# Kernel tuning notes

Measured on AMD Instinct MI355X. Metric: run time of the kernel, lower is better.

## Reference

```python
import jax, jax.numpy as jnp
import numpy as np

HID = 128
EDGE_FEAT = 4
NUM_G = 20
CUTOFF = 10.0
N_NODES = 20000
N_EDGES = 640000


def setup_inputs() -> dict:
    key = jax.random.key(0)
    ks = jax.random.split(key, 20)
    s = 0.02
    in_e = 2 * HID + EDGE_FEAT + NUM_G  # 280
    inp = {
        "h": jax.random.normal(ks[0], (N_NODES, HID), jnp.float32),
        "x": jax.random.normal(ks[1], (N_NODES, 3), jnp.float32),
        "edge_attr": jax.random.normal(ks[2], (N_EDGES, EDGE_FEAT), jnp.float32),
        "edge_index": jax.random.randint(ks[3], (2, N_EDGES), 0, N_NODES, jnp.int32),
        "mask_ligand": jax.random.randint(ks[4], (N_NODES,), 0, 2, jnp.int32),
        # edge_mlp: 2 linear layers, silu after both (act_last=True)
        "W_e1": jax.random.normal(ks[5], (in_e, HID), jnp.float32) * s,
        "b_e1": jnp.zeros((HID,), jnp.float32),
        "W_e2": jax.random.normal(ks[6], (HID, HID), jnp.float32) * s,
        "b_e2": jnp.zeros((HID,), jnp.float32),
        # edge gate: Linear(hidden,1) + sigmoid
        "W_g": jax.random.normal(ks[7], (HID, 1), jnp.float32) * s,
        "b_g": jnp.zeros((1,), jnp.float32),
        # node_mlp: Linear -> silu -> Linear (no act last)
        "W_n1": jax.random.normal(ks[8], (2 * HID, HID), jnp.float32) * s,
        "b_n1": jnp.zeros((HID,), jnp.float32),
        "W_n2": jax.random.normal(ks[9], (HID, HID), jnp.float32) * s,
        "b_n2": jnp.zeros((HID,), jnp.float32),
        # x_mlp: Linear -> silu -> Linear(no bias, tiny init) -> tanh
        "W_x1": jax.random.normal(ks[10], (HID, HID), jnp.float32) * s,
        "b_x1": jnp.zeros((HID,), jnp.float32),
        "W_x2": jax.random.normal(ks[11], (HID, 1), jnp.float32) * 0.001,
    }
    return inp


def reference(h, x, edge_attr, W_e1, b_e1, W_e2, b_e2, W_g, b_g,
              W_n1, b_n1, W_n2, b_n2, W_x1, b_x1, W_x2,
              edge_index, mask_ligand):
    src, dst = edge_index[0], edge_index[1]
    rel = x[dst] - x[src]                                # [E,3]
    d2 = jnp.sum(rel * rel, axis=-1, keepdims=True)     # [E,1]
    r = jnp.sqrt(d2 + 1e-8)
    # Gaussian smearing RBF
    offset = jnp.linspace(0.0, CUTOFF, NUM_G)
    coeff = -0.5 / (offset[1] - offset[0]) ** 2
    d_feat = jnp.exp(coeff * (r - offset) ** 2)          # [E,NUM_G]
    m_in = jnp.concatenate([h[dst], h[src], d_feat, edge_attr], axis=-1)
    m = jax.nn.silu(m_in @ W_e1 + b_e1)
    m = jax.nn.silu(m @ W_e2 + b_e2)
    g = jax.nn.sigmoid(m @ W_g + b_g)                    # [E,1]
    msg = m * g
    agg = jnp.zeros((h.shape[0], HID), msg.dtype).at[dst].add(msg)
    nm = jax.nn.silu(jnp.concatenate([agg, h], axis=-1) @ W_n1 + b_n1)
    h_out = h + (nm @ W_n2 + b_n2)
    coef = jnp.tanh(jax.nn.silu(m @ W_x1 + b_x1) @ W_x2)  # [E,1]
    vec = rel / (r + 1.0) * coef
    dx = jnp.zeros_like(x).at[dst].add(vec.astype(x.dtype))
    x_out = x + dx * mask_ligand.astype(x.dtype)[:, None]
    return (h_out, x_out)
```

## Files before the change

### kernel.cpp

```cpp
#include <hip/hip_runtime.h>
#include <hip/hip_bf16.h>
#include <math.h>

#define HID 128
#define NUM_G 20
#define EF 4
#define NN 20000
#define NE 640000
#define KN1 256
#define TS 136

typedef __attribute__((ext_vector_type(8))) short short8;
typedef __attribute__((ext_vector_type(4))) short short4v;
typedef __attribute__((ext_vector_type(4))) float floatx4;
typedef __attribute__((ext_vector_type(4))) unsigned int uintx4;

__device__ __forceinline__ float silu_f(float v){
    return v * __builtin_amdgcn_rcpf(1.0f + __expf(-v));
}
__device__ __forceinline__ float sigm_f(float v){
    return __builtin_amdgcn_rcpf(1.0f + __expf(-v));
}
__device__ __forceinline__ float tanh_f(float v){
    return 1.0f - 2.0f * __builtin_amdgcn_rcpf(1.0f + __expf(2.0f * v));
}
__device__ __forceinline__ unsigned short f2bf(float v){
    unsigned int u = __float_as_uint(v);
    u = (u + 0x7fffu + ((u >> 16) & 1u)) >> 16;
    return (unsigned short)u;
}
__device__ __forceinline__ float bf2f(unsigned short u){
    return __uint_as_float(((unsigned int)u) << 16);
}
__device__ __forceinline__ unsigned int pk2(float a, float b){
    __hip_bfloat162 h = __float22bfloat162_rn(make_float2(a, b));
    return *(unsigned int*)&h;
}
__device__ __forceinline__ float2 up2(unsigned int u){
    __hip_bfloat162 h = *(__hip_bfloat162*)&u;
    return __bfloat1622float2(h);
}

__global__ __launch_bounds__(320) void prep_hist_kernel(
    const float* __restrict__ W_e1, const float* __restrict__ W_e2,
    const float* __restrict__ W_x1, const float* __restrict__ W_n1,
    const float* __restrict__ W_n2,
    unsigned short* __restrict__ WT1d, unsigned short* __restrict__ WT1s,
    unsigned short* __restrict__ WT1r,
    unsigned short* __restrict__ WT_e2, unsigned short* __restrict__ WT_x1,
    unsigned short* __restrict__ WT_n1, unsigned short* __restrict__ WT_n2,
    const int* __restrict__ edge_index, int* __restrict__ counts)
{
    int t = threadIdx.x;
    if (blockIdx.x < 128) {
        int n = blockIdx.x;
        if (t < HID) {
            WT1d[n*HID + t] = f2bf(W_e1[t*HID + n]);
            WT1s[n*HID + t] = f2bf(W_e1[(HID+t)*HID + n]);
            WT_e2[n*HID + t] = f2bf(W_e2[t*HID + n]);
            WT_x1[n*HID + t] = f2bf(W_x1[t*HID + n]);
            WT_n2[n*HID + t] = f2bf(W_n2[t*HID + n]);
        }
        if (t < 32) WT1r[n*32 + t] = (t < NUM_G+EF) ? f2bf(W_e1[(256+t)*HID + n]) : (unsigned short)0;
        if (t < KN1) WT_n1[n*KN1 + t] = f2bf(W_n1[t*HID + n]);
    } else {
        int e = (blockIdx.x - 128) * 320 + t;
        atomicAdd(&counts[edge_index[NE + e]], 1);
    }
}

__global__ __launch_bounds__(1024) void scan_kernel(
    const int* __restrict__ counts, int* __restrict__ cursor)
{
    __shared__ int part[1024];
    const int t = threadIdx.x;
    const int CH = (NN + 1023) / 1024;
    int base = t * CH;
    int s = 0;
    for (int i = 0; i < CH; ++i) { int idx = base + i; if (idx < NN) s += counts[idx]; }
    part[t] = s; __syncthreads();
    for (int off = 1; off < 1024; off <<= 1) {
        int v = (t >= off) ? part[t - off] : 0;
        __syncthreads();
        part[t] += v;
        __syncthreads();
    }
    int run = (t == 0) ? 0 : part[t - 1];
    for (int i = 0; i < CH; ++i) {
        int idx = base + i;
        if (idx < NN) { cursor[idx] = run; run += counts[idx]; }
    }
}

#define PD_BLOCKS ((NN + 63) / 64)
__global__ __launch_bounds__(256) void build_pd_kernel(
    const int* __restrict__ edge_index, const float* __restrict__ x,
    const float* __restrict__ edge_attr, int* __restrict__ cursor,
    int2* __restrict__ pair2, float4* __restrict__ geom4,
    unsigned short* __restrict__ attrb,
    const float* __restrict__ h, const float* __restrict__ b_e1,
    const unsigned short* __restrict__ WT1d, const unsigned short* __restrict__ WT1s,
    unsigned short* __restrict__ PD, unsigned short* __restrict__ PS)
{
    __shared__ __align__(16) unsigned short T[4][16*TS];

    if (blockIdx.x >= PD_BLOCKS) {
        int e = (blockIdx.x - PD_BLOCKS) * 256 + threadIdx.x;
        int s = edge_index[e];
        int d = edge_index[NE + e];
        int pos = atomicAdd(&cursor[d], 1);
        float rx = x[d*3+0] - x[s*3+0];
        float ry = x[d*3+1] - x[s*3+1];
        float rz = x[d*3+2] - x[s*3+2];
        float r  = sqrtf(rx*rx + ry*ry + rz*rz + 1e-8f);
        pair2[pos] = make_int2(s, d);
        geom4[pos] = make_float4(rx, ry, rz, r);
        short4v a;
        #pragma unroll
        for (int j = 0; j < 4; ++j) a[j] = (short)f2bf(edge_attr[(size_t)e*EF + j]);
        *(short4v*)(attrb + (size_t)pos*4) = a;
        return;
    }

    const int wv   = threadIdx.x >> 6;
    const int lane = threadIdx.x & 63;
    const int quad = lane >> 4;
    const int l15  = lane & 15;
    int node = blockIdx.x * 64 + wv * 16 + l15;
    if (node >= NN) node = NN - 1;
    unsigned short* Tw = &T[wv][0];

    short8 ah[4];
    #pragma unroll
    for (int kc = 0; kc < 4; ++kc) {
        const float* p = h + (size_t)node*HID + kc*32 + quad*8;
        float4 f0 = *(const float4*)(p);
        float4 f1 = *(const float4*)(p + 4);
        uintx4 u;
        u[0] = pk2(f0.x, f0.y); u[1] = pk2(f0.z, f0.w);
        u[2] = pk2(f1.x, f1.y); u[3] = pk2(f1.z, f1.w);
        ah[kc] = __builtin_bit_cast(short8, u);
    }

    floatx4 ad[8], as[8];
    #pragma unroll
    for (int t = 0; t < 8; ++t) { ad[t] = (floatx4){0,0,0,0}; as[t] = (floatx4){0,0,0,0}; }
    #pragma unroll
    for (int kc = 0; kc < 4; ++kc) {
        #pragma unroll
        for (int t = 0; t < 8; ++t) {
            short8 bd = *(const short8*)(WT1d + (size_t)(t*16+l15)*HID + kc*32 + quad*8);
            short8 bs = *(const short8*)(WT1s + (size_t)(t*16+l15)*HID + kc*32 + quad*8);
            ad[t] = __builtin_amdgcn_mfma_f32_16x16x32_bf16(ah[kc], bd, ad[t], 0, 0, 0);
            as[t] = __builtin_amdgcn_mfma_f32_16x16x32_bf16(ah[kc], bs, as[t], 0, 0, 0);
        }
    }
    #pragma unroll
    for (int t = 0; t < 8; ++t) {
        int col = t*16 + l15;
        float bv = b_e1[col];
        #pragma unroll
        for (int i = 0; i < 4; ++i)
            Tw[(quad*4+i)*TS + col] = f2bf(ad[t][i] + bv);
    }
    __builtin_amdgcn_wave_barrier();
    #pragma unroll
    for (int kc = 0; kc < 4; ++kc)
        *(short8*)(PD + (size_t)node*HID + kc*32 + quad*8) =
            *(const short8*)(&Tw[l15*TS + kc*32 + quad*8]);
    __builtin_amdgcn_wave_barrier();
    #pragma unroll
    for (int t = 0; t < 8; ++t) {
        int col = t*16 + l15;
        #pragma unroll
        for (int i = 0; i < 4; ++i)
            Tw[(quad*4+i)*TS + col] = f2bf(as[t][i]);
    }
    __builtin_amdgcn_wave_barrier();
    #pragma unroll
    for (int kc = 0; kc < 4; ++kc)
        *(short8*)(PS + (size_t)node*HID + kc*32 + quad*8) =
            *(const short8*)(&Tw[l15*TS + kc*32 + quad*8]);
}

__global__ __launch_bounds__(128, 3) void egnn_edge_mfma(
    const int2* __restrict__ pair2, const float4* __restrict__ geom4,
    const unsigned short* __restrict__ attrb,
    const unsigned short* __restrict__ PD, const unsigned short* __restrict__ PS,
    const unsigned short* __restrict__ WT1r,
    const unsigned short* __restrict__ WT_e2,
    const unsigned short* __restrict__ WT_x1,
    const float* __restrict__ b_e2,
    const float* __restrict__ W_g,  const float* __restrict__ b_g,
    const float* __restrict__ b_x1, const float* __restrict__ W_x2,
    float* __restrict__ agg, float* __restrict__ dxv)
{
    __shared__ __align__(16) unsigned short T[2][32*TS];
    __shared__ int   s_dst[2][33];
    __shared__ float s_g[2][32];
    __shared__ float s_vec[2][96];

    const int wv   = threadIdx.x >> 6;
    const int lane = threadIdx.x & 63;
    const int quad = lane >> 4;
    const int l15  = lane & 15;
    const int bid  = (int)(blockIdx.x & 7) * 1250 + (int)(blockIdx.x >> 3);
    const int e0   = (bid * 2 + wv) * 32;

    unsigned short* Tw = &T[wv][0];

    int   sreg = 0, dreg = 0;
    float rxr = 0.f, ryr = 0.f, rzr = 0.f, rreg = 0.f;
    if (lane < 32) {
        int2  p = pair2[e0 + lane];
        float4 g = geom4[e0 + lane];
        sreg = p.x; dreg = p.y;
        rxr = g.x; ryr = g.y; rzr = g.z; rreg = g.w;
        s_dst[wv][lane] = dreg;
    }
    if (lane == 32) s_dst[wv][32] = -1;

    const int   nd0 = __shfl(dreg, l15);
    const int   ns0 = __shfl(sreg, l15);
    const float rr0 = __shfl(rreg, l15);
    const int   nd1 = __shfl(dreg, 16 + l15);
    const int   ns1 = __shfl(sreg, 16 + l15);
    const float rr1 = __shfl(rreg, 16 + l15);

    short8 pdv0[4], psv0[4], pdv1[4], psv1[4];
    #pragma unroll
    for (int kc = 0; kc < 4; ++kc) {
        pdv0[kc] = *(const short8*)(PD + (size_t)nd0*HID + kc*32 + quad*8);
        psv0[kc] = *(const short8*)(PS + (size_t)ns0*HID + kc*32 + quad*8);
        pdv1[kc] = *(const short8*)(PD + (size_t)nd1*HID + kc*32 + quad*8);
        psv1[kc] = *(const short8*)(PS + (size_t)ns1*HID + kc*32 + quad*8);
    }

    short8 ar0, ar1;
    {
        const float step  = 10.0f / 19.0f;
        const float coeff = -0.5f / (step*step);
        uintx4 u0, u1;
        #pragma unroll
        for (int jp = 0; jp < 4; ++jp) {
            float v[4];
            #pragma unroll
            for (int half = 0; half < 2; ++half) {
                float rr = half ? rr1 : rr0;
                int rowbase = e0 + (half ? 16 : 0) + l15;
                #pragma unroll
                for (int q = 0; q < 2; ++q) {
                    int col = quad*8 + jp*2 + q;
                    float val = 0.f;
                    if (col < NUM_G) {
                        float d = rr - step*(float)col;
                        val = __expf(coeff*d*d);
                    } else if (col < NUM_G+EF) {
                        val = bf2f(attrb[(size_t)rowbase*4 + (col-NUM_G)]);
                    }
                    v[half*2 + q] = val;
                }
            }
            u0[jp] = pk2(v[0], v[1]);
            u1[jp] = pk2(v[2], v[3]);
        }
        ar0 = __builtin_bit_cast(short8, u0);
        ar1 = __builtin_bit_cast(short8, u1);
    }

    floatx4 acc0[8], acc1[8];
    #pragma unroll
    for (int t = 0; t < 8; ++t) { acc0[t] = (floatx4){0,0,0,0}; acc1[t] = (floatx4){0,0,0,0}; }
    #pragma unroll
    for (int t = 0; t < 8; ++t) {
        short8 b = *(const short8*)(WT1r + (size_t)(t*16+l15)*32 + quad*8);
        acc0[t] = __builtin_amdgcn_mfma_f32_16x16x32_bf16(ar0, b, acc0[t], 0, 0, 0);
        acc1[t] = __builtin_amdgcn_mfma_f32_16x16x32_bf16(ar1, b, acc1[t], 0, 0, 0);
    }
    #pragma unroll
    for (int t = 0; t < 8; ++t) {
        int col = t*16 + l15;
        #pragma unroll
        for (int i = 0; i < 4; i += 2) {
            unsigned int u0 = pk2(acc0[t][i], acc0[t][i+1]);
            unsigned int u1 = pk2(acc1[t][i], acc1[t][i+1]);
            Tw[(quad*4+i)*TS + col]        = (unsigned short)u0;
            Tw[(quad*4+i+1)*TS + col]      = (unsigned short)(u0 >> 16);
            Tw[(16+quad*4+i)*TS + col]     = (unsigned short)u1;
            Tw[(16+quad*4+i+1)*TS + col]   = (unsigned short)(u1 >> 16);
        }
    }
    __builtin_amdgcn_wave_barrier();

    short8 a2[8];
    #pragma unroll
    for (int kc = 0; kc < 4; ++kc) {
        uintx4 rv0 = __builtin_bit_cast(uintx4, *(const short8*)(&Tw[l15*TS + kc*32 + quad*8]));
        uintx4 rv1 = __builtin_bit_cast(uintx4, *(const short8*)(&Tw[(16+l15)*TS + kc*32 + quad*8]));
        uintx4 pu0 = __builtin_bit_cast(uintx4, pdv0[kc]);
        uintx4 su0 = __builtin_bit_cast(uintx4, psv0[kc]);
        uintx4 pu1 = __builtin_bit_cast(uintx4, pdv1[kc]);
        uintx4 su1 = __builtin_bit_cast(uintx4, psv1[kc]);
        uintx4 o0, o1;
        #pragma unroll
        for (int w = 0; w < 4; ++w) {
            float2 p0 = up2(pu0[w]), s0 = up2(su0[w]), r0 = up2(rv0[w]);
            float2 p1 = up2(pu1[w]), s1 = up2(su1[w]), r1 = up2(rv1[w]);
            o0[w] = pk2(silu_f(p0.x + s0.x + r0.x), silu_f(p0.y + s0.y + r0.y));
            o1[w] = pk2(silu_f(p1.x + s1.x + r1.x), silu_f(p1.y + s1.y + r1.y));
        }
        a2[kc]   = __builtin_bit_cast(short8, o0);
        a2[4+kc] = __builtin_bit_cast(short8, o1);
    }
    __builtin_amdgcn_wave_barrier();

    #pragma unroll
    for (int t = 0; t < 8; ++t) { acc0[t] = (floatx4){0,0,0,0}; acc1[t] = (floatx4){0,0,0,0}; }
    #pragma unroll
    for (int kc = 0; kc < 4; ++kc) {
        #pragma unroll
        for (int t = 0; t < 8; ++t) {
            short8 b = *(const short8*)(WT_e2 + (size_t)(t*16+l15)*HID + kc*32 + quad*8);
            acc0[t] = __builtin_amdgcn_mfma_f32_16x16x32_bf16(a2[kc],   b, acc0[t], 0, 0, 0);
            acc1[t] = __builtin_amdgcn_mfma_f32_16x16x32_bf16(a2[4+kc], b, acc1[t], 0, 0, 0);
        }
    }
    {
        float gp0[4] = {0,0,0,0}, gp1[4] = {0,0,0,0};
        #pragma unroll
        for (int t = 0; t < 8; ++t) {
            int col = t*16 + l15;
            float bv = b_e2[col];
            float wgv = W_g[col];
            #pragma unroll
            for (int i = 0; i < 4; i += 2) {
                float m20a = silu_f(acc0[t][i]   + bv);
                float m20b = silu_f(acc0[t][i+1] + bv);
                float m21a = silu_f(acc1[t][i]   + bv);
                float m21b = silu_f(acc1[t][i+1] + bv);
                gp0[i] += m20a * wgv; gp0[i+1] += m20b * wgv;
                gp1[i] += m21a * wgv; gp1[i+1] += m21b * wgv;
                unsigned int u0 = pk2(m20a, m20b);
                unsigned int u1 = pk2(m21a, m21b);
                Tw[(quad*4+i)*TS + col]      = (unsigned short)u0;
                Tw[(quad*4+i+1)*TS + col]    = (unsigned short)(u0 >> 16);
                Tw[(16+quad*4+i)*TS + col]   = (unsigned short)u1;
                Tw[(16+quad*4+i+1)*TS + col] = (unsigned short)(u1 >> 16);
            }
        }
        const float bg0 = b_g[0];
        #pragma unroll
        for (int i = 0; i < 4; ++i) {
            gp0[i] += __shfl_xor(gp0[i], 1); gp0[i] += __shfl_xor(gp0[i], 2);
            gp0[i] += __shfl_xor(gp0[i], 4); gp0[i] += __shfl_xor(gp0[i], 8);
            gp1[i] += __shfl_xor(gp1[i], 1); gp1[i] += __shfl_xor(gp1[i], 2);
            gp1[i] += __shfl_xor(gp1[i], 4); gp1[i] += __shfl_xor(gp1[i], 8);
        }
        if (l15 == 0) {
            #pragma unroll
            for (int i = 0; i < 4; ++i) {
                s_g[wv][quad*4 + i]      = sigm_f(gp0[i] + bg0);
                s_g[wv][16 + quad*4 + i] = sigm_f(gp1[i] + bg0);
            }
        }
    }
    __builtin_amdgcn_wave_barrier();

    #pragma unroll
    for (int kc = 0; kc < 4; ++kc) {
        a2[kc]   = *(const short8*)(&Tw[l15*TS + kc*32 + quad*8]);
        a2[4+kc] = *(const short8*)(&Tw[(16+l15)*TS + kc*32 + quad*8]);
    }
    #pragma unroll
    for (int t = 0; t < 8; ++t) { acc0[t] = (floatx4){0,0,0,0}; acc1[t] = (floatx4){0,0,0,0}; }
    #pragma unroll
    for (int kc = 0; kc < 4; ++kc) {
        #pragma unroll
        for (int t = 0; t < 8; ++t) {
            short8 b = *(const short8*)(WT_x1 + (size_t)(t*16+l15)*HID + kc*32 + quad*8);
            acc0[t] = __builtin_amdgcn_mfma_f32_16x16x32_bf16(a2[kc],   b, acc0[t], 0, 0, 0);
            acc1[t] = __builtin_amdgcn_mfma_f32_16x16x32_bf16(a2[4+kc], b, acc1[t], 0, 0, 0);
        }
    }

    {
        float am0 = 0.f, am1 = 0.f;
        #pragma unroll
        for (int r = 0; r < 32; ++r) {
            unsigned int pv = *(const unsigned int*)(&Tw[r*TS + lane*2]);
            float gr = s_g[wv][r];
            float2 f = up2(pv);
            am0 += f.x * gr;
            am1 += f.y * gr;
            int dr = s_dst[wv][r];
            if (dr != s_dst[wv][r+1]) {
                atomicAdd(&agg[(size_t)dr*HID + lane*2],     am0);
                atomicAdd(&agg[(size_t)dr*HID + lane*2 + 1], am1);
                am0 = 0.f; am1 = 0.f;
            }
        }
    }

    {
        float cp0[4] = {0,0,0,0}, cp1[4] = {0,0,0,0};
        #pragma unroll
        for (int t = 0; t < 8; ++t) {
            int col = t*16 + l15;
            float bv = b_x1[col];
            float wx = W_x2[col];
            #pragma unroll
            for (int i = 0; i < 4; ++i) {
                cp0[i] += silu_f(acc0[t][i] + bv) * wx;
                cp1[i] += silu_f(acc1[t][i] + bv) * wx;
            }
        }
        #pragma unroll
        for (int i = 0; i < 4; ++i) {
            cp0[i] += __shfl_xor(cp0[i], 1); cp0[i] += __shfl_xor(cp0[i], 2);
            cp0[i] += __shfl_xor(cp0[i], 4); cp0[i] += __shfl_xor(cp0[i], 8);
            cp1[i] += __shfl_xor(cp1[i], 1); cp1[i] += __shfl_xor(cp1[i], 2);
            cp1[i] += __shfl_xor(cp1[i], 4); cp1[i] += __shfl_xor(cp1[i], 8);
        }
        if (l15 < 3) {
            #pragma unroll
            for (int i = 0; i < 4; ++i) {
                int r0 = quad*4 + i;
                int r1 = 16 + quad*4 + i;
                float relc0 = (l15 == 0) ? __shfl(rxr, r0) : ((l15 == 1) ? __shfl(ryr, r0) : __shfl(rzr, r0));
                float relc1 = (l15 == 0) ? __shfl(rxr, r1) : ((l15 == 1) ? __shfl(ryr, r1) : __shfl(rzr, r1));
                float rv0 = __shfl(rreg, r0);
                float rv1 = __shfl(rreg, r1);
                s_vec[wv][r0*3 + l15] = relc0 * __builtin_amdgcn_rcpf(rv0 + 1.0f) * tanh_f(cp0[i]);
                s_vec[wv][r1*3 + l15] = relc1 * __builtin_amdgcn_rcpf(rv1 + 1.0f) * tanh_f(cp1[i]);
            }
        }
    }
    __builtin_amdgcn_wave_barrier();

    if (lane < 3) {
        float a = 0.f;
        #pragma unroll
        for (int r = 0; r < 32; ++r) {
            a += s_vec[wv][r*3 + lane];
            int dr = s_dst[wv][r];
            if (dr != s_dst[wv][r+1]) {
                atomicAdd(&dxv[(size_t)dr*3 + lane], a);
                a = 0.f;
            }
        }
    }
}

__global__ __launch_bounds__(64, 4) void egnn_node_mfma(
    const float* __restrict__ h, const float* __restrict__ x,
    const int* __restrict__ mask,
    const float* __restrict__ agg, const float* __restrict__ dxv,
    const unsigned short* __restrict__ WT_n1, const float* __restrict__ b_n1,
    const unsigned short* __restrict__ WT_n2, const float* __restrict__ b_n2,
    float* __restrict__ h_out, float* __restrict__ x_out)
{
    __shared__ __align__(16) unsigned short T[16*TS];

    const int lane = threadIdx.x;
    const int quad = lane >> 4;
    const int l15  = lane & 15;
    const int n0   = blockIdx.x * 16;

    if (lane < 48) {
        int r = lane / 3, c = lane % 3;
        int n = n0 + r;
        x_out[n*3 + c] = x[n*3 + c] + dxv[n*3 + c] * (float)mask[n];
    }

    const int node = n0 + l15;
    short8 a1[8];
    #pragma unroll
    for (int kc = 0; kc < 4; ++kc) {
        const float* p = agg + (size_t)node*HID + kc*32 + quad*8;
        float4 f0 = *(const float4*)(p);
        float4 f1 = *(const float4*)(p + 4);
        uintx4 u;
        u[0] = pk2(f0.x, f0.y); u[1] = pk2(f0.z, f0.w);
        u[2] = pk2(f1.x, f1.y); u[3] = pk2(f1.z, f1.w);
        a1[kc] = __builtin_bit_cast(short8, u);
    }
    #pragma unroll
    for (int kc = 0; kc < 4; ++kc) {
        const float* p = h + (size_t)node*HID + kc*32 + quad*8;
        float4 f0 = *(const float4*)(p);
        float4 f1 = *(const float4*)(p + 4);
        uintx4 u;
        u[0] = pk2(f0.x, f0.y); u[1] = pk2(f0.z, f0.w);
        u[2] = pk2(f1.x, f1.y); u[3] = pk2(f1.z, f1.w);
        a1[4+kc] = __builtin_bit_cast(short8, u);
    }

    floatx4 acc[8];
    #pragma unroll
    for (int t = 0; t < 8; ++t) acc[t] = (floatx4){0,0,0,0};
    #pragma unroll
    for (int kc = 0; kc < 8; ++kc) {
        #pragma unroll
        for (int t = 0; t < 8; ++t) {
            short8 b = *(const short8*)(WT_n1 + (size_t)(t*16+l15)*KN1 + kc*32 + quad*8);
            acc[t] = __builtin_amdgcn_mfma_f32_16x16x32_bf16(a1[kc], b, acc[t], 0, 0, 0);
        }
    }
    #pragma unroll
    for (int t = 0; t < 8; ++t) {
        int col = t*16 + l15;
        float bv = b_n1[col];
        #pragma unroll
        for (int i = 0; i < 4; i += 2) {
            unsigned int u = pk2(silu_f(acc[t][i] + bv), silu_f(acc[t][i+1] + bv));
            T[(quad*4+i)*TS + col]   = (unsigned short)u;
            T[(quad*4+i+1)*TS + col] = (unsigned short)(u >> 16);
        }
    }
    __builtin_amdgcn_wave_barrier();

    short8 a2[4];
    #pragma unroll
    for (int kc = 0; kc < 4; ++kc)
        a2[kc] = *(const short8*)(&T[l15*TS + kc*32 + quad*8]);
    #pragma unroll
    for (int t = 0; t < 8; ++t) acc[t] = (floatx4){0,0,0,0};
    #pragma unroll
    for (int kc = 0; kc < 4; ++kc) {
        #pragma unroll
        for (int t = 0; t < 8; ++t) {
            short8 b = *(const short8*)(WT_n2 + (size_t)(t*16+l15)*HID + kc*32 + quad*8);
            acc[t] = __builtin_amdgcn_mfma_f32_16x16x32_bf16(a2[kc], b, acc[t], 0, 0, 0);
        }
    }
    #pragma unroll
    for (int t = 0; t < 8; ++t) {
        int col = t*16 + l15;
        float bv = b_n2[col];
        #pragma unroll
        for (int i = 0; i < 4; ++i) {
            int n = n0 + quad*4 + i;
            h_out[(size_t)n*HID + col] = h[(size_t)n*HID + col] + acc[t][i] + bv;
        }
    }
}

extern "C" void kernel_launch(void* const* d_in, const int* in_sizes, int n_in,
                              void* d_out, int out_size, void* d_ws, size_t ws_size,
                              hipStream_t stream) {
    const float* h          = (const float*)d_in[0];
    const float* x          = (const float*)d_in[1];
    const float* edge_attr  = (const float*)d_in[2];
    const int*   edge_index = (const int*)  d_in[3];
    const int*   mask       = (const int*)  d_in[4];
    const float* W_e1 = (const float*)d_in[5];
    const float* b_e1 = (const float*)d_in[6];
    const float* W_e2 = (const float*)d_in[7];
    const float* b_e2 = (const float*)d_in[8];
    const float* W_g  = (const float*)d_in[9];
    const float* b_g  = (const float*)d_in[10];
    const float* W_n1 = (const float*)d_in[11];
    const float* b_n1 = (const float*)d_in[12];
    const float* W_n2 = (const float*)d_in[13];
    const float* b_n2 = (const float*)d_in[14];
    const float* W_x1 = (const float*)d_in[15];
    const float* b_x1 = (const float*)d_in[16];
    const float* W_x2 = (const float*)d_in[17];

    char* ws = (char*)d_ws;
    float* agg = (float*)ws;                       ws += (size_t)NN*HID*4;
    float* dxv = (float*)ws;                       ws += (size_t)NN*3*4;
    int*   counts = (int*)ws;                      ws += (size_t)NN*4;
    int*   cursor = (int*)ws;                      ws += (size_t)NN*4;
    int2*  pair2  = (int2*)ws;                     ws += (size_t)NE*8;
    float4* geom4 = (float4*)ws;                   ws += (size_t)NE*16;
    unsigned short* attrb = (unsigned short*)ws;   ws += (size_t)NE*4*2;
    unsigned short* PD    = (unsigned short*)ws;   ws += (size_t)NN*HID*2;
    unsigned short* PS    = (unsigned short*)ws;   ws += (size_t)NN*HID*2;
    unsigned short* WT1d  = (unsigned short*)ws;   ws += (size_t)HID*HID*2;
    unsigned short* WT1s  = (unsigned short*)ws;   ws += (size_t)HID*HID*2;
    unsigned short* WT1r  = (unsigned short*)ws;   ws += (size_t)HID*32*2;
    unsigned short* WT_e2 = (unsigned short*)ws;   ws += (size_t)HID*HID*2;
    unsigned short* WT_x1 = (unsigned short*)ws;   ws += (size_t)HID*HID*2;
    unsigned short* WT_n1 = (unsigned short*)ws;   ws += (size_t)HID*KN1*2;
    unsigned short* WT_n2 = (unsigned short*)ws;   ws += (size_t)HID*HID*2;

    hipMemsetAsync(agg, 0, ((size_t)NN*HID + (size_t)NN*3)*sizeof(float), stream);
    hipMemsetAsync(counts, 0, (size_t)NN*sizeof(int), stream);

    prep_hist_kernel<<<128 + NE/320, 320, 0, stream>>>(
        W_e1, W_e2, W_x1, W_n1, W_n2,
        WT1d, WT1s, WT1r, WT_e2, WT_x1, WT_n1, WT_n2,
        edge_index, counts);

    scan_kernel<<<1, 1024, 0, stream>>>(counts, cursor);

    build_pd_kernel<<<PD_BLOCKS + NE/256, 256, 0, stream>>>(
        edge_index, x, edge_attr, cursor, pair2, geom4, attrb,
        h, b_e1, WT1d, WT1s, PD, PS);

    egnn_edge_mfma<<<NE/64, 128, 0, stream>>>(
        pair2, geom4, attrb, PD, PS, WT1r, WT_e2, WT_x1,
        b_e2, W_g, b_g, b_x1, W_x2, agg, dxv);

    float* h_out = (float*)d_out;
    float* x_out = h_out + (size_t)NN*HID;

    egnn_node_mfma<<<NN/16, 64, 0, stream>>>(
        h, x, mask, agg, dxv, WT_n1, b_n1, WT_n2, b_n2, h_out, x_out);
}
```

Measured before the change: 494.0 us.

## Swap MFMA operands for row-major outputs, XOR-swizzle LDS, fold biases into accumulators

Every MFMA now takes the weight as the A operand and the activation as B. Each lane therefore holds four consecutive output columns of one row, so results can be packed into 64-bit bf16 stores. The LDS staging tiles drop their padded stride and use an XOR swizzle on 16-byte chunks to avoid bank conflicts. Biases, and the residual h in the node MLP, are preloaded into the accumulators. The gate and coef reductions now need only two cross-quad shuffles. The per-edge dst-change detection moves from shared memory to a wave ballot, and s_setprio is raised around the MFMA loops. Together these cut LDS traffic, scalar stores and shuffle work, but the operand swap changes the accumulator layout, and the risk is in the index arithmetic.

```diff
diff --git a/kernel.cpp b/kernel.cpp
--- a/kernel.cpp
+++ b/kernel.cpp
@@ -8,7 +8,6 @@
 #define NN 20000
 #define NE 640000
 #define KN1 256
-#define TS 136
 
 typedef __attribute__((ext_vector_type(8))) short short8;
 typedef __attribute__((ext_vector_type(4))) short short4v;
@@ -35,6 +34,9 @@
 __device__ __forceinline__ unsigned int pk2(float a, float b){
     __hip_bfloat162 h = __float22bfloat162_rn(make_float2(a, b));
     return *(unsigned int*)&h;
+}
+__device__ __forceinline__ unsigned long long pk4(float a, float b, float c, float d){
+    return (unsigned long long)pk2(a, b) | ((unsigned long long)pk2(c, d) << 32);
 }
 __device__ __forceinline__ float2 up2(unsigned int u){
     __hip_bfloat162 h = *(__hip_bfloat162*)&u;
@@ -102,8 +104,6 @@
     const unsigned short* __restrict__ WT1d, const unsigned short* __restrict__ WT1s,
     unsigned short* __restrict__ PD, unsigned short* __restrict__ PS)
 {
-    __shared__ __align__(16) unsigned short T[4][16*TS];
-
     if (blockIdx.x >= PD_BLOCKS) {
         int e = (blockIdx.x - PD_BLOCKS) * 256 + threadIdx.x;
         int s = edge_index[e];
@@ -128,7 +128,6 @@
     const int l15  = lane & 15;
     int node = blockIdx.x * 64 + wv * 16 + l15;
     if (node >= NN) node = NN - 1;
-    unsigned short* Tw = &T[wv][0];
 
     short8 ah[4];
     #pragma unroll
@@ -142,45 +141,30 @@
         ah[kc] = __builtin_bit_cast(short8, u);
     }
 
-    floatx4 ad[8], as[8];
-    #pragma unroll
-    for (int t = 0; t < 8; ++t) { ad[t] = (floatx4){0,0,0,0}; as[t] = (floatx4){0,0,0,0}; }
+    floatx4 ad[8], as8[8];
+    #pragma unroll
+    for (int t = 0; t < 8; ++t) {
+        float4 bb = *(const float4*)(b_e1 + t*16 + quad*4);
+        ad[t]  = (floatx4){bb.x, bb.y, bb.z, bb.w};
+        as8[t] = (floatx4){0.f, 0.f, 0.f, 0.f};
+    }
     #pragma unroll
     for (int kc = 0; kc < 4; ++kc) {
         #pragma unroll
         for (int t = 0; t < 8; ++t) {
             short8 bd = *(const short8*)(WT1d + (size_t)(t*16+l15)*HID + kc*32 + quad*8);
             short8 bs = *(const short8*)(WT1s + (size_t)(t*16+l15)*HID + kc*32 + quad*8);
-            ad[t] = __builtin_amdgcn_mfma_f32_16x16x32_bf16(ah[kc], bd, ad[t], 0, 0, 0);
-            as[t] = __builtin_amdgcn_mfma_f32_16x16x32_bf16(ah[kc], bs, as[t], 0, 0, 0);
-        }
-    }
-    #pragma unroll
-    for (int t = 0; t < 8; ++t) {
-        int col = t*16 + l15;
-        float bv = b_e1[col];
-        #pragma unroll
-        for (int i = 0; i < 4; ++i)
-            Tw[(quad*4+i)*TS + col] = f2bf(ad[t][i] + bv);
-    }
-    __builtin_amdgcn_wave_barrier();
-    #pragma unroll
-    for (int kc = 0; kc < 4; ++kc)
-        *(short8*)(PD + (size_t)node*HID + kc*32 + quad*8) =
-            *(const short8*)(&Tw[l15*TS + kc*32 + quad*8]);
-    __builtin_amdgcn_wave_barrier();
-    #pragma unroll
-    for (int t = 0; t < 8; ++t) {
-        int col = t*16 + l15;
-        #pragma unroll
-        for (int i = 0; i < 4; ++i)
-            Tw[(quad*4+i)*TS + col] = f2bf(as[t][i]);
-    }
-    __builtin_amdgcn_wave_barrier();
-    #pragma unroll
-    for (int kc = 0; kc < 4; ++kc)
-        *(short8*)(PS + (size_t)node*HID + kc*32 + quad*8) =
-            *(const short8*)(&Tw[l15*TS + kc*32 + quad*8]);
+            ad[t]  = __builtin_amdgcn_mfma_f32_16x16x32_bf16(bd, ah[kc], ad[t], 0, 0, 0);
+            as8[t] = __builtin_amdgcn_mfma_f32_16x16x32_bf16(bs, ah[kc], as8[t], 0, 0, 0);
+        }
+    }
+    #pragma unroll
+    for (int t = 0; t < 8; ++t) {
+        *(unsigned long long*)(PD + (size_t)node*HID + t*16 + quad*4) =
+            pk4(ad[t][0], ad[t][1], ad[t][2], ad[t][3]);
+        *(unsigned long long*)(PS + (size_t)node*HID + t*16 + quad*4) =
+            pk4(as8[t][0], as8[t][1], as8[t][2], as8[t][3]);
+    }
 }
 
 __global__ __launch_bounds__(128, 3) void egnn_edge_mfma(
@@ -195,8 +179,7 @@
     const float* __restrict__ b_x1, const float* __restrict__ W_x2,
     float* __restrict__ agg, float* __restrict__ dxv)
 {
-    __shared__ __align__(16) unsigned short T[2][32*TS];
-    __shared__ int   s_dst[2][33];
+    __shared__ __align__(16) unsigned short T[2][32*HID];
     __shared__ float s_g[2][32];
     __shared__ float s_vec[2][96];
 
@@ -207,7 +190,8 @@
     const int bid  = (int)(blockIdx.x & 7) * 1250 + (int)(blockIdx.x >> 3);
     const int e0   = (bid * 2 + wv) * 32;
 
-    unsigned short* Tw = &T[wv][0];
+    char* Tb = (char*)&T[wv][0];
+    const int rsw = (l15 & 7) << 4;
 
     int   sreg = 0, dreg = 0;
     float rxr = 0.f, ryr = 0.f, rzr = 0.f, rreg = 0.f;
@@ -216,9 +200,10 @@
         float4 g = geom4[e0 + lane];
         sreg = p.x; dreg = p.y;
         rxr = g.x; ryr = g.y; rzr = g.z; rreg = g.w;
-        s_dst[wv][lane] = dreg;
-    }
-    if (lane == 32) s_dst[wv][32] = -1;
+    }
+    int nxt = __shfl(dreg, lane + 1);
+    const unsigned int bmask =
+        (unsigned int)__ballot(lane < 32 && (lane == 31 || dreg != nxt));
 
     const int   nd0 = __shfl(dreg, l15);
     const int   ns0 = __shfl(sreg, l15);
@@ -274,29 +259,25 @@
     #pragma unroll
     for (int t = 0; t < 8; ++t) {
         short8 b = *(const short8*)(WT1r + (size_t)(t*16+l15)*32 + quad*8);
-        acc0[t] = __builtin_amdgcn_mfma_f32_16x16x32_bf16(ar0, b, acc0[t], 0, 0, 0);
-        acc1[t] = __builtin_amdgcn_mfma_f32_16x16x32_bf16(ar1, b, acc1[t], 0, 0, 0);
-    }
-    #pragma unroll
-    for (int t = 0; t < 8; ++t) {
-        int col = t*16 + l15;
-        #pragma unroll
-        for (int i = 0; i < 4; i += 2) {
-            unsigned int u0 = pk2(acc0[t][i], acc0[t][i+1]);
-            unsigned int u1 = pk2(acc1[t][i], acc1[t][i+1]);
-            Tw[(quad*4+i)*TS + col]        = (unsigned short)u0;
-            Tw[(quad*4+i+1)*TS + col]      = (unsigned short)(u0 >> 16);
-            Tw[(16+quad*4+i)*TS + col]     = (unsigned short)u1;
-            Tw[(16+quad*4+i+1)*TS + col]   = (unsigned short)(u1 >> 16);
-        }
+        acc0[t] = __builtin_amdgcn_mfma_f32_16x16x32_bf16(b, ar0, acc0[t], 0, 0, 0);
+        acc1[t] = __builtin_amdgcn_mfma_f32_16x16x32_bf16(b, ar1, acc1[t], 0, 0, 0);
+    }
+    #pragma unroll
+    for (int t = 0; t < 8; ++t) {
+        int bc = (t*16 + quad*4) * 2;
+        *(unsigned long long*)(Tb + l15*256      + (bc ^ rsw)) =
+            pk4(acc0[t][0], acc0[t][1], acc0[t][2], acc0[t][3]);
+        *(unsigned long long*)(Tb + (16+l15)*256 + (bc ^ rsw)) =
+            pk4(acc1[t][0], acc1[t][1], acc1[t][2], acc1[t][3]);
     }
     __builtin_amdgcn_wave_barrier();
 
     short8 a2[8];
     #pragma unroll
     for (int kc = 0; kc < 4; ++kc) {
-        uintx4 rv0 = __builtin_bit_cast(uintx4, *(const short8*)(&Tw[l15*TS + kc*32 + quad*8]));
-        uintx4 rv1 = __builtin_bit_cast(uintx4, *(const short8*)(&Tw[(16+l15)*TS + kc*32 + quad*8]));
+        int bc = (kc*32 + quad*8) * 2;
+        uintx4 rv0 = __builtin_bit_cast(uintx4, *(const short8*)(Tb + l15*256      + (bc ^ rsw)));
+        uintx4 rv1 = __builtin_bit_cast(uintx4, *(const short8*)(Tb + (16+l15)*256 + (bc ^ rsw)));
         uintx4 pu0 = __builtin_bit_cast(uintx4, pdv0[kc]);
         uintx4 su0 = __builtin_bit_cast(uintx4, psv0[kc]);
         uintx4 pu1 = __builtin_bit_cast(uintx4, pdv1[kc]);
@@ -315,85 +296,82 @@
     __builtin_amdgcn_wave_barrier();
 
     #pragma unroll
-    for (int t = 0; t < 8; ++t) { acc0[t] = (floatx4){0,0,0,0}; acc1[t] = (floatx4){0,0,0,0}; }
+    for (int t = 0; t < 8; ++t) {
+        float4 bb = *(const float4*)(b_e2 + t*16 + quad*4);
+        acc0[t] = (floatx4){bb.x, bb.y, bb.z, bb.w};
+        acc1[t] = acc0[t];
+    }
+    __builtin_amdgcn_s_setprio(1);
     #pragma unroll
     for (int kc = 0; kc < 4; ++kc) {
         #pragma unroll
         for (int t = 0; t < 8; ++t) {
             short8 b = *(const short8*)(WT_e2 + (size_t)(t*16+l15)*HID + kc*32 + quad*8);
-            acc0[t] = __builtin_amdgcn_mfma_f32_16x16x32_bf16(a2[kc],   b, acc0[t], 0, 0, 0);
-            acc1[t] = __builtin_amdgcn_mfma_f32_16x16x32_bf16(a2[4+kc], b, acc1[t], 0, 0, 0);
-        }
-    }
+            acc0[t] = __builtin_amdgcn_mfma_f32_16x16x32_bf16(b, a2[kc],   acc0[t], 0, 0, 0);
+            acc1[t] = __builtin_amdgcn_mfma_f32_16x16x32_bf16(b, a2[4+kc], acc1[t], 0, 0, 0);
+        }
+    }
+    __builtin_amdgcn_s_setprio(0);
     {
-        float gp0[4] = {0,0,0,0}, gp1[4] = {0,0,0,0};
-        #pragma unroll
-        for (int t = 0; t < 8; ++t) {
-            int col = t*16 + l15;
-            float bv = b_e2[col];
-            float wgv = W_g[col];
-            #pragma unroll
-            for (int i = 0; i < 4; i += 2) {
-                float m20a = silu_f(acc0[t][i]   + bv);
-                float m20b = silu_f(acc0[t][i+1] + bv);
-                float m21a = silu_f(acc1[t][i]   + bv);
-                float m21b = silu_f(acc1[t][i+1] + bv);
-                gp0[i] += m20a * wgv; gp0[i+1] += m20b * wgv;
-                gp1[i] += m21a * wgv; gp1[i+1] += m21b * wgv;
-                unsigned int u0 = pk2(m20a, m20b);
-                unsigned int u1 = pk2(m21a, m21b);
-                Tw[(quad*4+i)*TS + col]      = (unsigned short)u0;
-                Tw[(quad*4+i+1)*TS + col]    = (unsigned short)(u0 >> 16);
-                Tw[(16+quad*4+i)*TS + col]   = (unsigned short)u1;
-                Tw[(16+quad*4+i+1)*TS + col] = (unsigned short)(u1 >> 16);
-            }
-        }
-        const float bg0 = b_g[0];
-        #pragma unroll
-        for (int i = 0; i < 4; ++i) {
-            gp0[i] += __shfl_xor(gp0[i], 1); gp0[i] += __shfl_xor(gp0[i], 2);
-            gp0[i] += __shfl_xor(gp0[i], 4); gp0[i] += __shfl_xor(gp0[i], 8);
-            gp1[i] += __shfl_xor(gp1[i], 1); gp1[i] += __shfl_xor(gp1[i], 2);
-            gp1[i] += __shfl_xor(gp1[i], 4); gp1[i] += __shfl_xor(gp1[i], 8);
-        }
-        if (l15 == 0) {
-            #pragma unroll
-            for (int i = 0; i < 4; ++i) {
-                s_g[wv][quad*4 + i]      = sigm_f(gp0[i] + bg0);
-                s_g[wv][16 + quad*4 + i] = sigm_f(gp1[i] + bg0);
-            }
+        float gp0 = 0.f, gp1 = 0.f;
+        #pragma unroll
+        for (int t = 0; t < 8; ++t) {
+            float4 wg = *(const float4*)(W_g + t*16 + quad*4);
+            float m0 = silu_f(acc0[t][0]), m1 = silu_f(acc0[t][1]);
+            float m2v = silu_f(acc0[t][2]), m3 = silu_f(acc0[t][3]);
+            float n0v = silu_f(acc1[t][0]), n1 = silu_f(acc1[t][1]);
+            float n2 = silu_f(acc1[t][2]),  n3 = silu_f(acc1[t][3]);
+            gp0 += m0*wg.x + m1*wg.y + m2v*wg.z + m3*wg.w;
+            gp1 += n0v*wg.x + n1*wg.y + n2*wg.z + n3*wg.w;
+            int bc = (t*16 + quad*4) * 2;
+            *(unsigned long long*)(Tb + l15*256      + (bc ^ rsw)) = pk4(m0, m1, m2v, m3);
+            *(unsigned long long*)(Tb + (16+l15)*256 + (bc ^ rsw)) = pk4(n0v, n1, n2, n3);
+        }
+        gp0 += __shfl_xor(gp0, 16); gp0 += __shfl_xor(gp0, 32);
+        gp1 += __shfl_xor(gp1, 16); gp1 += __shfl_xor(gp1, 32);
+        if (lane < 16) {
+            const float bg0 = b_g[0];
+            s_g[wv][l15]      = sigm_f(gp0 + bg0);
+            s_g[wv][16 + l15] = sigm_f(gp1 + bg0);
         }
     }
     __builtin_amdgcn_wave_barrier();
 
     #pragma unroll
     for (int kc = 0; kc < 4; ++kc) {
-        a2[kc]   = *(const short8*)(&Tw[l15*TS + kc*32 + quad*8]);
-        a2[4+kc] = *(const short8*)(&Tw[(16+l15)*TS + kc*32 + quad*8]);
-    }
-    #pragma unroll
-    for (int t = 0; t < 8; ++t) { acc0[t] = (floatx4){0,0,0,0}; acc1[t] = (floatx4){0,0,0,0}; }
+        int bc = (kc*32 + quad*8) * 2;
+        a2[kc]   = *(const short8*)(Tb + l15*256      + (bc ^ rsw));
+        a2[4+kc] = *(const short8*)(Tb + (16+l15)*256 + (bc ^ rsw));
+    }
+    #pragma unroll
+    for (int t = 0; t < 8; ++t) {
+        float4 bb = *(const float4*)(b_x1 + t*16 + quad*4);
+        acc0[t] = (floatx4){bb.x, bb.y, bb.z, bb.w};
+        acc1[t] = acc0[t];
+    }
+    __builtin_amdgcn_s_setprio(1);
     #pragma unroll
     for (int kc = 0; kc < 4; ++kc) {
         #pragma unroll
         for (int t = 0; t < 8; ++t) {
             short8 b = *(const short8*)(WT_x1 + (size_t)(t*16+l15)*HID + kc*32 + quad*8);
-            acc0[t] = __builtin_amdgcn_mfma_f32_16x16x32_bf16(a2[kc],   b, acc0[t], 0, 0, 0);
-            acc1[t] = __builtin_amdgcn_mfma_f32_16x16x32_bf16(a2[4+kc], b, acc1[t], 0, 0, 0);
-        }
-    }
+            acc0[t] = __builtin_amdgcn_mfma_f32_16x16x32_bf16(b, a2[kc],   acc0[t], 0, 0, 0);
+            acc1[t] = __builtin_amdgcn_mfma_f32_16x16x32_bf16(b, a2[4+kc], acc1[t], 0, 0, 0);
+        }
+    }
+    __builtin_amdgcn_s_setprio(0);
 
     {
         float am0 = 0.f, am1 = 0.f;
         #pragma unroll
         for (int r = 0; r < 32; ++r) {
-            unsigned int pv = *(const unsigned int*)(&Tw[r*TS + lane*2]);
+            unsigned int pv = *(const unsigned int*)(Tb + r*256 + ((lane*4) ^ ((r&7)<<4)));
             float gr = s_g[wv][r];
             float2 f = up2(pv);
             am0 += f.x * gr;
             am1 += f.y * gr;
-            int dr = s_dst[wv][r];
-            if (dr != s_dst[wv][r+1]) {
+            if (bmask & (1u << r)) {
+                int dr = __shfl(dreg, r);
                 atomicAdd(&agg[(size_t)dr*HID + lane*2],     am0);
                 atomicAdd(&agg[(size_t)dr*HID + lane*2 + 1], am1);
                 am0 = 0.f; am1 = 0.f;
@@ -402,49 +380,40 @@
     }
 
     {
-        float cp0[4] = {0,0,0,0}, cp1[4] = {0,0,0,0};
-        #pragma unroll
-        for (int t = 0; t < 8; ++t) {
-            int col = t*16 + l15;
-            float bv = b_x1[col];
-            float wx = W_x2[col];
-            #pragma unroll
-            for (int i = 0; i < 4; ++i) {
-                cp0[i] += silu_f(acc0[t][i] + bv) * wx;
-                cp1[i] += silu_f(acc1[t][i] + bv) * wx;
-            }
-        }
-        #pragma unroll
-        for (int i = 0; i < 4; ++i) {
-            cp0[i] += __shfl_xor(cp0[i], 1); cp0[i] += __shfl_xor(cp0[i], 2);
-            cp0[i] += __shfl_xor(cp0[i], 4); cp0[i] += __shfl_xor(cp0[i], 8);
-            cp1[i] += __shfl_xor(cp1[i], 1); cp1[i] += __shfl_xor(cp1[i], 2);
-            cp1[i] += __shfl_xor(cp1[i], 4); cp1[i] += __shfl_xor(cp1[i], 8);
-        }
-        if (l15 < 3) {
-            #pragma unroll
-            for (int i = 0; i < 4; ++i) {
-                int r0 = quad*4 + i;
-                int r1 = 16 + quad*4 + i;
-                float relc0 = (l15 == 0) ? __shfl(rxr, r0) : ((l15 == 1) ? __shfl(ryr, r0) : __shfl(rzr, r0));
-                float relc1 = (l15 == 0) ? __shfl(rxr, r1) : ((l15 == 1) ? __shfl(ryr, r1) : __shfl(rzr, r1));
-                float rv0 = __shfl(rreg, r0);
-                float rv1 = __shfl(rreg, r1);
-                s_vec[wv][r0*3 + l15] = relc0 * __builtin_amdgcn_rcpf(rv0 + 1.0f) * tanh_f(cp0[i]);
-                s_vec[wv][r1*3 + l15] = relc1 * __builtin_amdgcn_rcpf(rv1 + 1.0f) * tanh_f(cp1[i]);
-            }
+        float cp0 = 0.f, cp1 = 0.f;
+        #pragma unroll
+        for (int t = 0; t < 8; ++t) {
+            float4 wx = *(const float4*)(W_x2 + t*16 + quad*4);
+            cp0 += silu_f(acc0[t][0])*wx.x + silu_f(acc0[t][1])*wx.y
+                 + silu_f(acc0[t][2])*wx.z + silu_f(acc0[t][3])*wx.w;
+            cp1 += silu_f(acc1[t][0])*wx.x + silu_f(acc1[t][1])*wx.y
+                 + silu_f(acc1[t][2])*wx.z + silu_f(acc1[t][3])*wx.w;
+        }
+        cp0 += __shfl_xor(cp0, 16); cp0 += __shfl_xor(cp0, 32);
+        cp1 += __shfl_xor(cp1, 16); cp1 += __shfl_xor(cp1, 32);
+        if (quad < 2) {
+            int el = quad*16 + l15;
+            float cp = (quad == 0) ? cp0 : cp1;
+            float co = tanh_f(cp);
+            float rx = __shfl(rxr, el), ry = __shfl(ryr, el), rz = __shfl(rzr, el);
+            float rv = __shfl(rreg, el);
+            float sc = __builtin_amdgcn_rcpf(rv + 1.0f) * co;
+            s_vec[wv][el*3 + 0] = rx * sc;
+            s_vec[wv][el*3 + 1] = ry * sc;
+            s_vec[wv][el*3 + 2] = rz * sc;
         }
     }
     __builtin_amdgcn_wave_barrier();
 
-    if (lane < 3) {
+    {
         float a = 0.f;
         #pragma unroll
         for (int r = 0; r < 32; ++r) {
-            a += s_vec[wv][r*3 + lane];
-            int dr = s_dst[wv][r];
-            if (dr != s_dst[wv][r+1]) {
-                atomicAdd(&dxv[(size_t)dr*3 + lane], a);
+            float vv = (lane < 3) ? s_vec[wv][r*3 + lane] : 0.f;
+            a += vv;
+            if (bmask & (1u << r)) {
+                int dr = __shfl(dreg, r);
+                if (lane < 3) atomicAdd(&dxv[(size_t)dr*3 + lane], a);
                 a = 0.f;
             }
         }
@@ -459,12 +428,14 @@
     const unsigned short* __restrict__ WT_n2, const float* __restrict__ b_n2,
     float* __restrict__ h_out, float* __restrict__ x_out)
 {
-    __shared__ __align__(16) unsigned short T[16*TS];
+    __shared__ __align__(16) unsigned short T[16*HID];
 
     const int lane = threadIdx.x;
     const int quad = lane >> 4;
     const int l15  = lane & 15;
     const int n0   = blockIdx.x * 16;
+    char* Tb = (char*)T;
+    const int rsw = (l15 & 7) << 4;
 
     if (lane < 48) {
         int r = lane / 3, c = lane % 3;
@@ -497,51 +468,49 @@
 
     floatx4 acc[8];
     #pragma unroll
-    for (int t = 0; t < 8; ++t) acc[t] = (floatx4){0,0,0,0};
+    for (int t = 0; t < 8; ++t) {
+        float4 bb = *(const float4*)(b_n1 + t*16 + quad*4);
+        acc[t] = (floatx4){bb.x, bb.y, bb.z, bb.w};
+    }
     #pragma unroll
     for (int kc = 0; kc < 8; ++kc) {
         #pragma unroll
         for (int t = 0; t < 8; ++t) {
             short8 b = *(const short8*)(WT_n1 + (size_t)(t*16+l15)*KN1 + kc*32 + quad*8);
-            acc[t] = __builtin_amdgcn_mfma_f32_16x16x32_bf16(a1[kc], b, acc[t], 0, 0, 0);
-        }
-    }
-    #pragma unroll
-    for (int t = 0; t < 8; ++t) {
-        int col = t*16 + l15;
-        float bv = b_n1[col];
-        #pragma unroll
-        for (int i = 0; i < 4; i += 2) {
-            unsigned int u = pk2(silu_f(acc[t][i] + bv), silu_f(acc[t][i+1] + bv));
-            T[(quad*4+i)*TS + col]   = (unsigned short)u;
-            T[(quad*4+i+1)*TS + col] = (unsigned short)(u >> 16);
-        }
+            acc[t] = __builtin_amdgcn_mfma_f32_16x16x32_bf16(b, a1[kc], acc[t], 0, 0, 0);
+        }
+    }
+    #pragma unroll
+    for (int t = 0; t < 8; ++t) {
+        int bc = (t*16 + quad*4) * 2;
+        *(unsigned long long*)(Tb + l15*256 + (bc ^ rsw)) =
+            pk4(silu_f(acc[t][0]), silu_f(acc[t][1]), silu_f(acc[t][2]), silu_f(acc[t][3]));
     }
     __builtin_amdgcn_wave_barrier();
 
     short8 a2[4];
     #pragma unroll
-    for (int kc = 0; kc < 4; ++kc)
-        a2[kc] = *(const short8*)(&T[l15*TS + kc*32 + quad*8]);
-    #pragma unroll
-    for (int t = 0; t < 8; ++t) acc[t] = (floatx4){0,0,0,0};
+    for (int kc = 0; kc < 4; ++kc) {
+        int bc = (kc*32 + quad*8) * 2;
+        a2[kc] = *(const short8*)(Tb + l15*256 + (bc ^ rsw));
+    }
+    #pragma unroll
+    for (int t = 0; t < 8; ++t) {
+        float4 hv = *(const float4*)(h + (size_t)node*HID + t*16 + quad*4);
+        float4 bb = *(const float4*)(b_n2 + t*16 + quad*4);
+        acc[t] = (floatx4){hv.x + bb.x, hv.y + bb.y, hv.z + bb.z, hv.w + bb.w};
+    }
     #pragma unroll
     for (int kc = 0; kc < 4; ++kc) {
         #pragma unroll
         for (int t = 0; t < 8; ++t) {
             short8 b = *(const short8*)(WT_n2 + (size_t)(t*16+l15)*HID + kc*32 + quad*8);
-            acc[t] = __builtin_amdgcn_mfma_f32_16x16x32_bf16(a2[kc], b, acc[t], 0, 0, 0);
-        }
-    }
-    #pragma unroll
-    for (int t = 0; t < 8; ++t) {
-        int col = t*16 + l15;
-        float bv = b_n2[col];
-        #pragma unroll
-        for (int i = 0; i < 4; ++i) {
-            int n = n0 + quad*4 + i;
-            h_out[(size_t)n*HID + col] = h[(size_t)n*HID + col] + acc[t][i] + bv;
-        }
+            acc[t] = __builtin_amdgcn_mfma_f32_16x16x32_bf16(b, a2[kc], acc[t], 0, 0, 0);
+        }
+    }
+    #pragma unroll
+    for (int t = 0; t < 8; ++t) {
+        *(floatx4*)(h_out + (size_t)node*HID + t*16 + quad*4) = acc[t];
     }
 }
 
```

New measurement: 458.3 us. -7.2%, faster.
